# Kernel tuning notes

Hardware: AMD Instinct MI355X
Metric: run time of the kernel (lower is better)

Reference implementation:

```python
import jax, jax.numpy as jnp
import numpy as np

D_MODEL = 1024
NUM_HEAD = 16
D_HEAD = D_MODEL // NUM_HEAD
D_FFN = 4096
EPS = 1e-6


def setup_inputs() -> dict:
    key = jax.random.key(0)
    ks = jax.random.split(key, 8)
    s = 0.02
    return {
        "x": jax.random.normal(ks[0], (2, 2048, D_MODEL), dtype=jnp.float32),
        "wq": jax.random.normal(ks[1], (D_MODEL, D_MODEL), dtype=jnp.float32) * s,
        "bq": jnp.zeros((D_MODEL,), jnp.float32),
        "ln1_a": jax.random.uniform(ks[2], (D_MODEL,), dtype=jnp.float32),
        "ln1_b": jnp.zeros((D_MODEL,), jnp.float32),
        "ln2_a": jax.random.uniform(ks[3], (D_MODEL,), dtype=jnp.float32),
        "ln2_b": jnp.zeros((D_MODEL,), jnp.float32),
        "w1": jax.random.normal(ks[4], (D_FFN, D_MODEL), dtype=jnp.float32) * s,
        "b1": jnp.zeros((D_FFN,), jnp.float32),
        "w2": jax.random.normal(ks[5], (D_MODEL, D_FFN), dtype=jnp.float32) * s,
        "b2": jnp.zeros((D_MODEL,), jnp.float32),
    }


def _laynorm(x, a, b):
    # torch.std is unbiased (ddof=1); original divides by (std + eps)
    mean = jnp.mean(x, axis=-1, keepdims=True)
    std = jnp.std(x, axis=-1, keepdims=True, ddof=1)
    return a * ((x - mean) / (std + EPS)) + b


def reference(x, wq, bq, ln1_a, ln1_b, ln2_a, ln2_b, w1, b1, w2, b2):
    B, S, D = x.shape
    # NOTE: original applies Wq to Q, K, and V (Wk/Wv unused); Wo never applied.
    h = x @ wq.T + bq                      # [B,S,D]
    h = h.reshape(B, S, NUM_HEAD, D_HEAD)  # q = k = v = h
    scale = 1.0 / jnp.sqrt(jnp.float32(D_HEAD))
    scores = jnp.einsum("bqhd,bkhd->bhqk", h, h) * scale  # [B,H,S,S]
    att = jax.nn.softmax(scores, axis=-1)
    att_out = jnp.einsum("bhqk,bkhd->bqhd", att, h).reshape(B, S, D)
    # dropout is identity at inference
    x1 = _laynorm(x + att_out, ln1_a, ln1_b)
    ffn = jax.nn.relu(x1 @ w1.T + b1) @ w2.T + b2
    return _laynorm(x1 + ffn, ln2_a, ln2_b)
```

## Files before the change

### kernel.cpp

```cpp
#include <hip/hip_runtime.h>

typedef __bf16 bf16v8 __attribute__((ext_vector_type(8)));
typedef float f32x4 __attribute__((ext_vector_type(4)));

#define AS1 __attribute__((address_space(1)))
#define AS3 __attribute__((address_space(3)))

__device__ __forceinline__ void gl_lds16(const void* g, void* s) {
  __builtin_amdgcn_global_load_lds((const AS1 void*)g, (AS3 void*)s, 16, 0, 0);
}

__device__ __forceinline__ unsigned short f2b(float f) {
  union { float f; unsigned u; } v; v.f = f;
  unsigned r = v.u + 0x7fffu + ((v.u >> 16) & 1u);
  return (unsigned short)(r >> 16);
}

__device__ __forceinline__ float bitsf(unsigned u) {
  union { unsigned u; float f; } v; v.u = u;
  return v.f;
}

__global__ __launch_bounds__(256) void cvt_bf16(const float* __restrict__ in,
                                                unsigned short* __restrict__ out, int n4) {
  int i = blockIdx.x * 256 + threadIdx.x;
  if (i < n4) {
    float4 v = *(const float4*)(in + (long)i * 4);
    ushort4 u = make_ushort4(f2b(v.x), f2b(v.y), f2b(v.z), f2b(v.w));
    *(ushort4*)(out + (long)i * 4) = u;
  }
}

template <int RELU, int SPLIT>
__global__ __launch_bounds__(512, 2) void gemm256p(const unsigned short* __restrict__ A,
                                                   const unsigned short* __restrict__ B,
                                                   const float* __restrict__ bias,
                                                   unsigned short* __restrict__ Cb,
                                                   int M, int N, int K, int Ks) {
  __shared__ unsigned short As[2][2][8192];
  __shared__ unsigned short Bs[2][2][8192];

  const int tid = threadIdx.x;
  const int wave = tid >> 6, lane = tid & 63;
  const int wr = wave >> 2, wc = wave & 3;
  const int g = lane >> 4, l15 = lane & 15;

  const int gx = gridDim.x;
  const int nwg = gx * gridDim.y;
  const int lin = blockIdx.y * gx + blockIdx.x;
  const int cpx = nwg >> 3;
  const int swz = (lin & 7) * cpx + (lin >> 3);
  const long m0 = (long)(swz / gx) * 256;
  const long n0 = (long)(swz % gx) * 256;
  const int kBase = blockIdx.z * Ks;

  const int srow = lane >> 2;
  const int schunk = ((lane & 3) ^ ((lane >> 3) & 3)) * 8;

  auto stA = [&](int buf, int kk, int kb) {
#pragma unroll
    for (int j = 0; j < 2; ++j) {
      const int seg = wave * 2 + j;
      gl_lds16(A + (m0 + seg * 16 + srow) * (long)K + kb + kk * 32 + schunk,
               &As[buf][kk][seg * 512]);
    }
  };
  auto stB = [&](int buf, int kk, int kb) {
#pragma unroll
    for (int j = 0; j < 2; ++j) {
      const int seg = wave * 2 + j;
      gl_lds16(B + (n0 + seg * 16 + srow) * (long)K + kb + kk * 32 + schunk,
               &Bs[buf][kk][seg * 512]);
    }
  };

  const int sel = (l15 >> 1) & 3;
  const int colA = (g ^ sel) << 3;

  f32x4 acc[8][4] = {};
  const int nt = Ks >> 6;

  stA(0, 0, kBase); stB(0, 0, kBase); stA(0, 1, kBase); stB(0, 1, kBase);
  asm volatile("s_waitcnt vmcnt(4)" ::: "memory");
  __builtin_amdgcn_s_barrier();

  int cur = 0;
  for (int t = 0; t < nt; ++t) {
    const bool pf = (t + 1 < nt);
    const int kbn = kBase + ((t + 1) << 6);
    bf16v8 af[8], b0, b1, b2, b3;

#pragma unroll
    for (int m = 0; m < 8; ++m)
      af[m] = *(const bf16v8*)&As[cur][0][(wr * 128 + m * 16 + l15) * 32 + colA];
    b0 = *(const bf16v8*)&Bs[cur][0][(wc * 64 + 0 * 16 + l15) * 32 + colA];
    b1 = *(const bf16v8*)&Bs[cur][0][(wc * 64 + 1 * 16 + l15) * 32 + colA];
    if (pf) stA(cur ^ 1, 0, kbn);
    __builtin_amdgcn_s_barrier();
    asm volatile("s_waitcnt lgkmcnt(0)" ::: "memory");
    __builtin_amdgcn_s_setprio(1);
#pragma unroll
    for (int m = 0; m < 8; ++m) {
      acc[m][0] = __builtin_amdgcn_mfma_f32_16x16x32_bf16(af[m], b0, acc[m][0], 0, 0, 0);
      acc[m][1] = __builtin_amdgcn_mfma_f32_16x16x32_bf16(af[m], b1, acc[m][1], 0, 0, 0);
    }
    __builtin_amdgcn_s_setprio(0);
    __builtin_amdgcn_s_barrier();

    b2 = *(const bf16v8*)&Bs[cur][0][(wc * 64 + 2 * 16 + l15) * 32 + colA];
    b3 = *(const bf16v8*)&Bs[cur][0][(wc * 64 + 3 * 16 + l15) * 32 + colA];
    if (pf) stB(cur ^ 1, 0, kbn);
    __builtin_amdgcn_s_barrier();
    asm volatile("s_waitcnt lgkmcnt(0)" ::: "memory");
    __builtin_amdgcn_s_setprio(1);
#pragma unroll
    for (int m = 0; m < 8; ++m) {
      acc[m][2] = __builtin_amdgcn_mfma_f32_16x16x32_bf16(af[m], b2, acc[m][2], 0, 0, 0);
      acc[m][3] = __builtin_amdgcn_mfma_f32_16x16x32_bf16(af[m], b3, acc[m][3], 0, 0, 0);
    }
    __builtin_amdgcn_s_setprio(0);
    if (pf) { asm volatile("s_waitcnt vmcnt(4)" ::: "memory"); }
    else    { asm volatile("s_waitcnt vmcnt(0)" ::: "memory"); }
    __builtin_amdgcn_s_barrier();

#pragma unroll
    for (int m = 0; m < 8; ++m)
      af[m] = *(const bf16v8*)&As[cur][1][(wr * 128 + m * 16 + l15) * 32 + colA];
    b0 = *(const bf16v8*)&Bs[cur][1][(wc * 64 + 0 * 16 + l15) * 32 + colA];
    b1 = *(const bf16v8*)&Bs[cur][1][(wc * 64 + 1 * 16 + l15) * 32 + colA];
    if (pf) stA(cur ^ 1, 1, kbn);
    __builtin_amdgcn_s_barrier();
    asm volatile("s_waitcnt lgkmcnt(0)" ::: "memory");
    __builtin_amdgcn_s_setprio(1);
#pragma unroll
    for (int m = 0; m < 8; ++m) {
      acc[m][0] = __builtin_amdgcn_mfma_f32_16x16x32_bf16(af[m], b0, acc[m][0], 0, 0, 0);
      acc[m][1] = __builtin_amdgcn_mfma_f32_16x16x32_bf16(af[m], b1, acc[m][1], 0, 0, 0);
    }
    __builtin_amdgcn_s_setprio(0);
    __builtin_amdgcn_s_barrier();

    b2 = *(const bf16v8*)&Bs[cur][1][(wc * 64 + 2 * 16 + l15) * 32 + colA];
    b3 = *(const bf16v8*)&Bs[cur][1][(wc * 64 + 3 * 16 + l15) * 32 + colA];
    if (pf) stB(cur ^ 1, 1, kbn);
    __builtin_amdgcn_s_barrier();
    asm volatile("s_waitcnt lgkmcnt(0)" ::: "memory");
    __builtin_amdgcn_s_setprio(1);
#pragma unroll
    for (int m = 0; m < 8; ++m) {
      acc[m][2] = __builtin_amdgcn_mfma_f32_16x16x32_bf16(af[m], b2, acc[m][2], 0, 0, 0);
      acc[m][3] = __builtin_amdgcn_mfma_f32_16x16x32_bf16(af[m], b3, acc[m][3], 0, 0, 0);
    }
    __builtin_amdgcn_s_setprio(0);
    if (pf) { asm volatile("s_waitcnt vmcnt(4)" ::: "memory"); }
    else    { asm volatile("s_waitcnt vmcnt(0)" ::: "memory"); }
    __builtin_amdgcn_s_barrier();

    cur ^= 1;
  }

  const long zoff = SPLIT ? (long)blockIdx.z * M * (long)N : 0;
#pragma unroll
  for (int m = 0; m < 8; ++m)
#pragma unroll
    for (int n = 0; n < 4; ++n) {
      long col = n0 + wc * 64 + n * 16 + l15;
      float bv = SPLIT ? 0.f : bias[col];
      long rowb = m0 + wr * 128 + m * 16 + g * 4;
#pragma unroll
      for (int i = 0; i < 4; ++i) {
        float v = acc[m][n][i] + bv;
        if (RELU) v = fmaxf(v, 0.f);
        Cb[zoff + (rowb + i) * (long)N + col] = f2b(v);
      }
    }
}

__global__ __launch_bounds__(256) void merge4_bias(const unsigned short* __restrict__ p,
                                                   const float* __restrict__ bias,
                                                   unsigned short* __restrict__ out) {
  const long PS = 4096L * 1024L;
  long i = ((long)blockIdx.x * 256 + threadIdx.x) * 8;
  int col = (int)(i & 1023);
  float4 b0 = *(const float4*)(bias + col);
  float4 b1 = *(const float4*)(bias + col + 4);
  float acc[8] = {b0.x, b0.y, b0.z, b0.w, b1.x, b1.y, b1.z, b1.w};
#pragma unroll
  for (int sp = 0; sp < 4; ++sp) {
    uint4 u = *(const uint4*)(p + sp * PS + i);
    unsigned r[4] = {u.x, u.y, u.z, u.w};
#pragma unroll
    for (int j = 0; j < 4; ++j) {
      acc[j * 2]     += bitsf(r[j] << 16);
      acc[j * 2 + 1] += bitsf(r[j] & 0xffff0000u);
    }
  }
  unsigned short res[8];
#pragma unroll
  for (int j = 0; j < 8; ++j) res[j] = f2b(acc[j]);
  *(uint4*)(out + i) = *(uint4*)res;
}

__global__ __launch_bounds__(512, 2) void attn_kernel(const unsigned short* __restrict__ h,
                                                      float* __restrict__ o) {
  const int id = blockIdx.y * 8 + blockIdx.x;
  const int bh = id & 31;
  const int b = bh >> 4, head = bh & 15;
  const int q0 = (id >> 5) * 256;
  const unsigned short* hb = h + (long)b * 2048 * 1024 + head * 64;

  __shared__ unsigned short smem[2 * 19712];

  const int tid = threadIdx.x, wave = tid >> 6, lane = tid & 63;
  const int grp = wave >> 2, wg = wave & 3;
  const int g = lane >> 4, l15 = lane & 15;
  const int vcb = wg * 16;
  unsigned short* Ks0 = smem + grp * 19712;
  unsigned short* VTb = Ks0 + 8192;

  for (int idx = wg * 64 + lane; idx < 16 * 72; idx += 256) {
    unsigned short v = (idx < 72) ? (unsigned short)0x3F80 : (unsigned short)0;
    VTb[64 * 72 + idx] = v;
    VTb[5760 + 64 * 72 + idx] = v;
  }

  const float C1 = 0.18033688011112042f;

  bf16v8 qf[4][2];
#pragma unroll
  for (int qt = 0; qt < 4; ++qt)
#pragma unroll
    for (int d = 0; d < 2; ++d) {
      bf16v8 q = *(const bf16v8*)(hb + (long)(q0 + wg * 64 + qt * 16 + l15) * 1024 + d * 32 + g * 8);
#pragma unroll
      for (int j = 0; j < 8; ++j) q[j] = (__bf16)((float)q[j] * C1);
      qf[qt][d] = q;
    }

  const int krow = lane >> 3;
  const int kcol = ((lane & 7) ^ (krow & 7)) << 3;

  const int kl = lane;
  const int vpos = ((kl >> 5) << 5) + (((kl & 15) >> 2) << 3) + (((kl >> 4) & 1) << 2) + (kl & 3);

#pragma unroll
  for (int s = 0; s < 2; ++s) {
    int seg = wg * 2 + s;
    gl_lds16(hb + (long)(grp * 64 + seg * 8 + krow) * 1024 + kcol, Ks0 + seg * 512);
  }
  uint4 va0, va1;
  {
    const unsigned short* vg = hb + (long)(grp * 64 + lane) * 1024 + vcb;
    va0 = *(const uint4*)vg;
    va1 = *(const uint4*)(vg + 8);
  }
  {
    unsigned short vv[16];
    *(uint4*)&vv[0] = va0;
    *(uint4*)&vv[8] = va1;
#pragma unroll
    for (int j = 0; j < 16; ++j) VTb[(vcb + j) * 72 + vpos] = vv[j];
  }
  __syncthreads();

  f32x4 accO[4][4] = {};
  f32x4 accL[4] = {};

  int cur = 0;
  for (int t = 0; t < 16; ++t) {
    if (t < 15) {
      const int k0n = ((t + 1) * 2 + grp) * 64;
#pragma unroll
      for (int s = 0; s < 2; ++s) {
        int seg = wg * 2 + s;
        gl_lds16(hb + (long)(k0n + seg * 8 + krow) * 1024 + kcol, Ks0 + (cur ^ 1) * 4096 + seg * 512);
      }
      const unsigned short* vg = hb + (long)(k0n + lane) * 1024 + vcb;
      va0 = *(const uint4*)vg;
      va1 = *(const uint4*)(vg + 8);
    }

    const unsigned short* Kc = Ks0 + cur * 4096;
    f32x4 sf[4][4] = {};
#pragma unroll
    for (int d = 0; d < 2; ++d) {
#pragma unroll
      for (int kt = 0; kt < 4; ++kt) {
        int r = kt * 16 + l15;
        bf16v8 kf = *(const bf16v8*)&Kc[r * 64 + ((((d << 2) + g) ^ (r & 7)) << 3)];
#pragma unroll
        for (int qt = 0; qt < 4; ++qt)
          sf[kt][qt] = __builtin_amdgcn_mfma_f32_16x16x32_bf16(kf, qf[qt][d], sf[kt][qt], 0, 0, 0);
      }
    }

    bf16v8 pa[4][2];
#pragma unroll
    for (int qt = 0; qt < 4; ++qt) {
      float pe[4][4];
#pragma unroll
      for (int kt = 0; kt < 4; ++kt)
#pragma unroll
        for (int i = 0; i < 4; ++i)
          pe[kt][i] = __builtin_amdgcn_exp2f(sf[kt][qt][i]);
#pragma unroll
      for (int i = 0; i < 4; ++i) {
        pa[qt][0][i]     = (__bf16)pe[0][i];
        pa[qt][0][i + 4] = (__bf16)pe[1][i];
        pa[qt][1][i]     = (__bf16)pe[2][i];
        pa[qt][1][i + 4] = (__bf16)pe[3][i];
      }
    }

    const unsigned short* VTc = VTb + cur * 5760;
#pragma unroll
    for (int ks = 0; ks < 2; ++ks) {
      bf16v8 vl = *(const bf16v8*)&VTc[(64 + l15) * 72 + ks * 32 + g * 8];
#pragma unroll
      for (int dt = 0; dt < 4; ++dt) {
        bf16v8 vf = *(const bf16v8*)&VTc[(dt * 16 + l15) * 72 + ks * 32 + g * 8];
#pragma unroll
        for (int qt = 0; qt < 4; ++qt)
          accO[qt][dt] = __builtin_amdgcn_mfma_f32_16x16x32_bf16(pa[qt][ks], vf, accO[qt][dt], 0, 0, 0);
      }
#pragma unroll
      for (int qt = 0; qt < 4; ++qt)
        accL[qt] = __builtin_amdgcn_mfma_f32_16x16x32_bf16(pa[qt][ks], vl, accL[qt], 0, 0, 0);
    }

    if (t < 15) {
      unsigned short vv[16];
      *(uint4*)&vv[0] = va0;
      *(uint4*)&vv[8] = va1;
      unsigned short* VTn = VTb + (cur ^ 1) * 5760;
#pragma unroll
      for (int j = 0; j < 16; ++j) VTn[(vcb + j) * 72 + vpos] = vv[j];
    }
    __syncthreads();
    cur ^= 1;
  }

  float* redO = (float*)smem;
  float* redL = (float*)smem + 16384;
  if (grp == 1) {
#pragma unroll
    for (int qt = 0; qt < 4; ++qt)
#pragma unroll
      for (int i = 0; i < 4; ++i) {
        int r = wg * 64 + qt * 16 + g * 4 + i;
#pragma unroll
        for (int dt = 0; dt < 4; ++dt)
          redO[r * 64 + dt * 16 + l15] = accO[qt][dt][i];
        if (l15 == 0) redL[r] = accL[qt][i];
      }
  }
  __syncthreads();
  if (grp == 0) {
#pragma unroll
    for (int qt = 0; qt < 4; ++qt)
#pragma unroll
      for (int i = 0; i < 4; ++i) {
        int r = wg * 64 + qt * 16 + g * 4 + i;
#pragma unroll
        for (int dt = 0; dt < 4; ++dt)
          accO[qt][dt][i] += redO[r * 64 + dt * 16 + l15];
        accL[qt][i] += redL[r];
      }
#pragma unroll
    for (int qt = 0; qt < 4; ++qt)
#pragma unroll
      for (int i = 0; i < 4; ++i) {
        float linv = 1.f / __shfl(accL[qt][i], lane & 48);
        long row = (long)b * 2048 + q0 + wg * 64 + qt * 16 + g * 4 + i;
#pragma unroll
        for (int dt = 0; dt < 4; ++dt)
          o[row * 1024 + head * 64 + dt * 16 + l15] = accO[qt][dt][i] * linv;
      }
  }
}

template <int WB>
__global__ __launch_bounds__(256) void ln_add(const float* __restrict__ xa,
                                              const float* __restrict__ xb,
                                              const float* __restrict__ g,
                                              const float* __restrict__ be,
                                              float* __restrict__ of,
                                              unsigned short* __restrict__ ob) {
  const long base = (long)blockIdx.x * 1024;
  const int t = threadIdx.x;
  float4 va = *(const float4*)(xa + base + t * 4);
  float4 vb = *(const float4*)(xb + base + t * 4);
  float v0 = va.x + vb.x, v1 = va.y + vb.y, v2 = va.z + vb.z, v3 = va.w + vb.w;
  float s = v0 + v1 + v2 + v3;
  float sq = v0 * v0 + v1 * v1 + v2 * v2 + v3 * v3;
#pragma unroll
  for (int m = 1; m < 64; m <<= 1) { s += __shfl_xor(s, m); sq += __shfl_xor(sq, m); }
  __shared__ float red[8];
  const int wave = t >> 6, lane = t & 63;
  if (lane == 0) { red[wave] = s; red[4 + wave] = sq; }
  __syncthreads();
  s = red[0] + red[1] + red[2] + red[3];
  sq = red[4] + red[5] + red[6] + red[7];
  float mean = s * (1.f / 1024.f);
  float var = fmaxf(sq - s * mean, 0.f) * (1.f / 1023.f);
  float inv = 1.f / (sqrtf(var) + 1e-6f);
  float4 gg = *(const float4*)(g + t * 4);
  float4 bb = *(const float4*)(be + t * 4);
  float y0 = gg.x * ((v0 - mean) * inv) + bb.x;
  float y1 = gg.y * ((v1 - mean) * inv) + bb.y;
  float y2 = gg.z * ((v2 - mean) * inv) + bb.z;
  float y3 = gg.w * ((v3 - mean) * inv) + bb.w;
  *(float4*)(of + base + t * 4) = make_float4(y0, y1, y2, y3);
  if (WB) {
    ushort4 u = make_ushort4(f2b(y0), f2b(y1), f2b(y2), f2b(y3));
    *(ushort4*)(ob + base + t * 4) = u;
  }
}

__global__ __launch_bounds__(256) void ln_add_red4(const float* __restrict__ xa,
                                                   const unsigned short* __restrict__ zp,
                                                   const float* __restrict__ bias,
                                                   const float* __restrict__ g,
                                                   const float* __restrict__ be,
                                                   float* __restrict__ of) {
  const long base = (long)blockIdx.x * 1024;
  const int t = threadIdx.x;
  const long PS = 4096L * 1024L;
  float4 va = *(const float4*)(xa + base + t * 4);
  float4 bz = *(const float4*)(bias + t * 4);
  float v0 = va.x + bz.x, v1 = va.y + bz.y, v2 = va.z + bz.z, v3 = va.w + bz.w;
#pragma unroll
  for (int sp = 0; sp < 4; ++sp) {
    uint2 u = *(const uint2*)(zp + sp * PS + base + t * 4);
    v0 += bitsf(u.x << 16);
    v1 += bitsf(u.x & 0xffff0000u);
    v2 += bitsf(u.y << 16);
    v3 += bitsf(u.y & 0xffff0000u);
  }
  float s = v0 + v1 + v2 + v3;
  float sq = v0 * v0 + v1 * v1 + v2 * v2 + v3 * v3;
#pragma unroll
  for (int m = 1; m < 64; m <<= 1) { s += __shfl_xor(s, m); sq += __shfl_xor(sq, m); }
  __shared__ float red[8];
  const int wave = t >> 6, lane = t & 63;
  if (lane == 0) { red[wave] = s; red[4 + wave] = sq; }
  __syncthreads();
  s = red[0] + red[1] + red[2] + red[3];
  sq = red[4] + red[5] + red[6] + red[7];
  float mean = s * (1.f / 1024.f);
  float var = fmaxf(sq - s * mean, 0.f) * (1.f / 1023.f);
  float inv = 1.f / (sqrtf(var) + 1e-6f);
  float4 gg = *(const float4*)(g + t * 4);
  float4 bb = *(const float4*)(be + t * 4);
  float y0 = gg.x * ((v0 - mean) * inv) + bb.x;
  float y1 = gg.y * ((v1 - mean) * inv) + bb.y;
  float y2 = gg.z * ((v2 - mean) * inv) + bb.z;
  float y3 = gg.w * ((v3 - mean) * inv) + bb.w;
  *(float4*)(of + base + t * 4) = make_float4(y0, y1, y2, y3);
}

extern "C" void kernel_launch(void* const* d_in, const int* in_sizes, int n_in,
                              void* d_out, int out_size, void* d_ws, size_t ws_size,
                              hipStream_t stream) {
  const float* x    = (const float*)d_in[0];
  const float* wq   = (const float*)d_in[1];
  const float* bq   = (const float*)d_in[2];
  const float* ln1a = (const float*)d_in[3];
  const float* ln1b = (const float*)d_in[4];
  const float* ln2a = (const float*)d_in[5];
  const float* ln2b = (const float*)d_in[6];
  const float* w1   = (const float*)d_in[7];
  const float* b1   = (const float*)d_in[8];
  const float* w2   = (const float*)d_in[9];
  const float* b2   = (const float*)d_in[10];
  float* out = (float*)d_out;

  char* ws = (char*)d_ws;
  const size_t MB = 1024 * 1024;
  unsigned short* xb  = (unsigned short*)(ws);
  unsigned short* wqb = (unsigned short*)(ws + 8 * MB);
  unsigned short* w1b = (unsigned short*)(ws + 10 * MB);
  unsigned short* w2b = (unsigned short*)(ws + 18 * MB);
  unsigned short* qp  = (unsigned short*)(ws + 26 * MB);
  unsigned short* yb  = (unsigned short*)(ws + 26 * MB);
  unsigned short* hb  = (unsigned short*)(ws + 58 * MB);
  float*          att = (float*)(ws + 66 * MB);
  unsigned short* zp  = (unsigned short*)(ws + 58 * MB);
  float*          x1f = (float*)(ws + 90 * MB);
  unsigned short* x1b = (unsigned short*)(ws + 106 * MB);

  cvt_bf16<<<4096, 256, 0, stream>>>(x, xb, 1048576);
  cvt_bf16<<<1024, 256, 0, stream>>>(wq, wqb, 262144);
  cvt_bf16<<<4096, 256, 0, stream>>>(w1, w1b, 1048576);
  cvt_bf16<<<4096, 256, 0, stream>>>(w2, w2b, 1048576);

  gemm256p<0, 1><<<dim3(4, 16, 4), 512, 0, stream>>>(xb, wqb, nullptr, qp,
                                                     4096, 1024, 1024, 256);
  merge4_bias<<<2048, 256, 0, stream>>>(qp, bq, hb);

  attn_kernel<<<dim3(8, 32), 512, 0, stream>>>(hb, att);

  ln_add<1><<<4096, 256, 0, stream>>>(x, att, ln1a, ln1b, x1f, x1b);

  gemm256p<1, 0><<<dim3(16, 16, 1), 512, 0, stream>>>(x1b, w1b, b1, yb,
                                                      4096, 4096, 1024, 1024);

  gemm256p<0, 1><<<dim3(4, 16, 4), 512, 0, stream>>>(yb, w2b, nullptr, zp,
                                                     4096, 1024, 4096, 1024);

  ln_add_red4<<<4096, 256, 0, stream>>>(x1f, zp, b2, ln2a, ln2b, out);
}
```

Measured before the change: 183.5 us.

## Deepen GEMM LDS pipeline to four 32-wide k-slots with three-ahead prefetch

Replaces the double-buffered 64-wide k tiles with a ring of four 32-wide LDS slots, prefetching three sub-tiles ahead instead of one. The goal is to keep more global-to-LDS loads in flight and hide global memory latency behind the MFMA work. The outer loop now steps 128 in k and is unrolled across the four slots, with vmcnt waits adjusted to the deeper queue. LDS footprint stays the same. The loop now assumes Ks is a multiple of 128, and the wait counts are harder to get right.

Measured after the change: 187.3 us. 2.1% more time.

```diff
diff --git a/kernel.cpp b/kernel.cpp
--- a/kernel.cpp
+++ b/kernel.cpp
@@ -31,14 +31,52 @@
   }
 }
 
+#define PHASE_ODD(SLOT, STAGE_STMT)                                                         \
+  {                                                                                         \
+    _Pragma("unroll")                                                                       \
+    for (int m = 0; m < 8; ++m)                                                             \
+      af[m] = *(const bf16v8*)&As4[SLOT][(wr * 128 + m * 16 + l15) * 32 + colA];            \
+    b0 = *(const bf16v8*)&Bs4[SLOT][(wc * 64 + 0 * 16 + l15) * 32 + colA];                  \
+    b1 = *(const bf16v8*)&Bs4[SLOT][(wc * 64 + 1 * 16 + l15) * 32 + colA];                  \
+    STAGE_STMT;                                                                             \
+    __builtin_amdgcn_s_barrier();                                                           \
+    asm volatile("s_waitcnt lgkmcnt(0)" ::: "memory");                                      \
+    __builtin_amdgcn_s_setprio(1);                                                          \
+    _Pragma("unroll")                                                                       \
+    for (int m = 0; m < 8; ++m) {                                                           \
+      acc[m][0] = __builtin_amdgcn_mfma_f32_16x16x32_bf16(af[m], b0, acc[m][0], 0, 0, 0);   \
+      acc[m][1] = __builtin_amdgcn_mfma_f32_16x16x32_bf16(af[m], b1, acc[m][1], 0, 0, 0);   \
+    }                                                                                       \
+    __builtin_amdgcn_s_setprio(0);                                                          \
+    __builtin_amdgcn_s_barrier();                                                           \
+  }
+
+#define PHASE_EVEN(SLOT, STAGE_STMT, WAIT_STMT)                                             \
+  {                                                                                         \
+    b2 = *(const bf16v8*)&Bs4[SLOT][(wc * 64 + 2 * 16 + l15) * 32 + colA];                  \
+    b3 = *(const bf16v8*)&Bs4[SLOT][(wc * 64 + 3 * 16 + l15) * 32 + colA];                  \
+    STAGE_STMT;                                                                             \
+    __builtin_amdgcn_s_barrier();                                                           \
+    asm volatile("s_waitcnt lgkmcnt(0)" ::: "memory");                                      \
+    __builtin_amdgcn_s_setprio(1);                                                          \
+    _Pragma("unroll")                                                                       \
+    for (int m = 0; m < 8; ++m) {                                                           \
+      acc[m][2] = __builtin_amdgcn_mfma_f32_16x16x32_bf16(af[m], b2, acc[m][2], 0, 0, 0);   \
+      acc[m][3] = __builtin_amdgcn_mfma_f32_16x16x32_bf16(af[m], b3, acc[m][3], 0, 0, 0);   \
+    }                                                                                       \
+    __builtin_amdgcn_s_setprio(0);                                                          \
+    WAIT_STMT;                                                                              \
+    __builtin_amdgcn_s_barrier();                                                           \
+  }
+
 template <int RELU, int SPLIT>
 __global__ __launch_bounds__(512, 2) void gemm256p(const unsigned short* __restrict__ A,
                                                    const unsigned short* __restrict__ B,
                                                    const float* __restrict__ bias,
                                                    unsigned short* __restrict__ Cb,
                                                    int M, int N, int K, int Ks) {
-  __shared__ unsigned short As[2][2][8192];
-  __shared__ unsigned short Bs[2][2][8192];
+  __shared__ unsigned short As4[4][8192];
+  __shared__ unsigned short Bs4[4][8192];
 
   const int tid = threadIdx.x;
   const int wave = tid >> 6, lane = tid & 63;
@@ -57,20 +95,18 @@
   const int srow = lane >> 2;
   const int schunk = ((lane & 3) ^ ((lane >> 3) & 3)) * 8;
 
-  auto stA = [&](int buf, int kk, int kb) {
+  auto stA4 = [&](int slot, int kb) {
 #pragma unroll
     for (int j = 0; j < 2; ++j) {
       const int seg = wave * 2 + j;
-      gl_lds16(A + (m0 + seg * 16 + srow) * (long)K + kb + kk * 32 + schunk,
-               &As[buf][kk][seg * 512]);
+      gl_lds16(A + (m0 + seg * 16 + srow) * (long)K + kb + schunk, &As4[slot][seg * 512]);
     }
   };
-  auto stB = [&](int buf, int kk, int kb) {
+  auto stB4 = [&](int slot, int kb) {
 #pragma unroll
     for (int j = 0; j < 2; ++j) {
       const int seg = wave * 2 + j;
-      gl_lds16(B + (n0 + seg * 16 + srow) * (long)K + kb + kk * 32 + schunk,
-               &Bs[buf][kk][seg * 512]);
+      gl_lds16(B + (n0 + seg * 16 + srow) * (long)K + kb + schunk, &Bs4[slot][seg * 512]);
     }
   };
 
@@ -78,85 +114,34 @@
   const int colA = (g ^ sel) << 3;
 
   f32x4 acc[8][4] = {};
-  const int nt = Ks >> 6;
-
-  stA(0, 0, kBase); stB(0, 0, kBase); stA(0, 1, kBase); stB(0, 1, kBase);
-  asm volatile("s_waitcnt vmcnt(4)" ::: "memory");
+  const int npair = Ks >> 7;
+
+  stA4(0, kBase);      stB4(0, kBase);
+  stA4(1, kBase + 32); stB4(1, kBase + 32);
+  stA4(2, kBase + 64); stB4(2, kBase + 64);
+  asm volatile("s_waitcnt vmcnt(8)" ::: "memory");
   __builtin_amdgcn_s_barrier();
 
-  int cur = 0;
-  for (int t = 0; t < nt; ++t) {
-    const bool pf = (t + 1 < nt);
-    const int kbn = kBase + ((t + 1) << 6);
+  for (int p = 0; p < npair; ++p) {
+    const int tb = kBase + (p << 7);
+    const int tbn = tb + 128;
+    const bool pf = (p + 1 < npair);
     bf16v8 af[8], b0, b1, b2, b3;
 
-#pragma unroll
-    for (int m = 0; m < 8; ++m)
-      af[m] = *(const bf16v8*)&As[cur][0][(wr * 128 + m * 16 + l15) * 32 + colA];
-    b0 = *(const bf16v8*)&Bs[cur][0][(wc * 64 + 0 * 16 + l15) * 32 + colA];
-    b1 = *(const bf16v8*)&Bs[cur][0][(wc * 64 + 1 * 16 + l15) * 32 + colA];
-    if (pf) stA(cur ^ 1, 0, kbn);
-    __builtin_amdgcn_s_barrier();
-    asm volatile("s_waitcnt lgkmcnt(0)" ::: "memory");
-    __builtin_amdgcn_s_setprio(1);
-#pragma unroll
-    for (int m = 0; m < 8; ++m) {
-      acc[m][0] = __builtin_amdgcn_mfma_f32_16x16x32_bf16(af[m], b0, acc[m][0], 0, 0, 0);
-      acc[m][1] = __builtin_amdgcn_mfma_f32_16x16x32_bf16(af[m], b1, acc[m][1], 0, 0, 0);
-    }
-    __builtin_amdgcn_s_setprio(0);
-    __builtin_amdgcn_s_barrier();
-
-    b2 = *(const bf16v8*)&Bs[cur][0][(wc * 64 + 2 * 16 + l15) * 32 + colA];
-    b3 = *(const bf16v8*)&Bs[cur][0][(wc * 64 + 3 * 16 + l15) * 32 + colA];
-    if (pf) stB(cur ^ 1, 0, kbn);
-    __builtin_amdgcn_s_barrier();
-    asm volatile("s_waitcnt lgkmcnt(0)" ::: "memory");
-    __builtin_amdgcn_s_setprio(1);
-#pragma unroll
-    for (int m = 0; m < 8; ++m) {
-      acc[m][2] = __builtin_amdgcn_mfma_f32_16x16x32_bf16(af[m], b2, acc[m][2], 0, 0, 0);
-      acc[m][3] = __builtin_amdgcn_mfma_f32_16x16x32_bf16(af[m], b3, acc[m][3], 0, 0, 0);
-    }
-    __builtin_amdgcn_s_setprio(0);
-    if (pf) { asm volatile("s_waitcnt vmcnt(4)" ::: "memory"); }
-    else    { asm volatile("s_waitcnt vmcnt(0)" ::: "memory"); }
-    __builtin_amdgcn_s_barrier();
-
-#pragma unroll
-    for (int m = 0; m < 8; ++m)
-      af[m] = *(const bf16v8*)&As[cur][1][(wr * 128 + m * 16 + l15) * 32 + colA];
-    b0 = *(const bf16v8*)&Bs[cur][1][(wc * 64 + 0 * 16 + l15) * 32 + colA];
-    b1 = *(const bf16v8*)&Bs[cur][1][(wc * 64 + 1 * 16 + l15) * 32 + colA];
-    if (pf) stA(cur ^ 1, 1, kbn);
-    __builtin_amdgcn_s_barrier();
-    asm volatile("s_waitcnt lgkmcnt(0)" ::: "memory");
-    __builtin_amdgcn_s_setprio(1);
-#pragma unroll
-    for (int m = 0; m < 8; ++m) {
-      acc[m][0] = __builtin_amdgcn_mfma_f32_16x16x32_bf16(af[m], b0, acc[m][0], 0, 0, 0);
-      acc[m][1] = __builtin_amdgcn_mfma_f32_16x16x32_bf16(af[m], b1, acc[m][1], 0, 0, 0);
-    }
-    __builtin_amdgcn_s_setprio(0);
-    __builtin_amdgcn_s_barrier();
-
-    b2 = *(const bf16v8*)&Bs[cur][1][(wc * 64 + 2 * 16 + l15) * 32 + colA];
-    b3 = *(const bf16v8*)&Bs[cur][1][(wc * 64 + 3 * 16 + l15) * 32 + colA];
-    if (pf) stB(cur ^ 1, 1, kbn);
-    __builtin_amdgcn_s_barrier();
-    asm volatile("s_waitcnt lgkmcnt(0)" ::: "memory");
-    __builtin_amdgcn_s_setprio(1);
-#pragma unroll
-    for (int m = 0; m < 8; ++m) {
-      acc[m][2] = __builtin_amdgcn_mfma_f32_16x16x32_bf16(af[m], b2, acc[m][2], 0, 0, 0);
-      acc[m][3] = __builtin_amdgcn_mfma_f32_16x16x32_bf16(af[m], b3, acc[m][3], 0, 0, 0);
-    }
-    __builtin_amdgcn_s_setprio(0);
-    if (pf) { asm volatile("s_waitcnt vmcnt(4)" ::: "memory"); }
-    else    { asm volatile("s_waitcnt vmcnt(0)" ::: "memory"); }
-    __builtin_amdgcn_s_barrier();
-
-    cur ^= 1;
+    PHASE_ODD (0, stA4(3, tb + 96));
+    PHASE_EVEN(0, stB4(3, tb + 96),
+               asm volatile("s_waitcnt vmcnt(8)" ::: "memory"));
+    PHASE_ODD (1, if (pf) stA4(0, tbn));
+    PHASE_EVEN(1, if (pf) stB4(0, tbn),
+               if (pf) { asm volatile("s_waitcnt vmcnt(8)" ::: "memory"); }
+               else    { asm volatile("s_waitcnt vmcnt(4)" ::: "memory"); });
+    PHASE_ODD (2, if (pf) stA4(1, tbn + 32));
+    PHASE_EVEN(2, if (pf) stB4(1, tbn + 32),
+               if (pf) { asm volatile("s_waitcnt vmcnt(8)" ::: "memory"); }
+               else    { asm volatile("s_waitcnt vmcnt(0)" ::: "memory"); });
+    PHASE_ODD (3, if (pf) stA4(2, tbn + 64));
+    PHASE_EVEN(3, if (pf) stB4(2, tbn + 64),
+               if (pf) { asm volatile("s_waitcnt vmcnt(8)" ::: "memory"); });
   }
 
   const long zoff = SPLIT ? (long)blockIdx.z * M * (long)N : 0;
```
